# Kernel optimization log

Measured on AMD Instinct MI355X. Metric: run time of the kernel, lower is better.

The kernel has to match this reference:

```python
import jax, jax.numpy as jnp
import numpy as np

B, N, DIM, H = 32, 3136, 768, 12
C = DIM // H  # head_dim = 64


def setup_inputs() -> dict:
    key = jax.random.key(0)
    k1, k2, k3, k4 = jax.random.split(key, 4)
    x = jax.random.normal(k1, (B, N, DIM), dtype=jnp.float32)
    # Linear weights stored as (in, out); qkv has no bias (qkv_bias=False)
    w_qkv = jax.random.normal(k2, (DIM, 3 * DIM), dtype=jnp.float32) * (1.0 / np.sqrt(DIM))
    w_proj = jax.random.normal(k3, (DIM, DIM), dtype=jnp.float32) * (1.0 / np.sqrt(DIM))
    b_proj = jax.random.normal(k4, (DIM,), dtype=jnp.float32) * 0.01
    return {"x": x, "w_qkv": w_qkv, "w_proj": w_proj, "b_proj": b_proj}


def reference(x, w_qkv, w_proj, b_proj):
    # qkv projection: [B,N,3*DIM] -> [3,B,H,N,C]
    qkv = (x @ w_qkv).reshape(B, N, 3, H, C).transpose(2, 0, 3, 1, 4)
    q, k, v = qkv[0], qkv[1], qkv[2]
    # Efficient (linear) attention: softmax q over channel dim, k over token dim
    q = jax.nn.softmax(q, axis=-1)                      # [B,H,N,C], softmax over C
    kt = jax.nn.softmax(k.transpose(0, 1, 3, 2), axis=-1)  # [B,H,C,N], softmax over N
    context = jnp.einsum('bhcn,bhnd->bhcd', kt, v)      # [B,H,C,C]
    out = jnp.einsum('bhnc,bhcd->bhnd', q, context)     # [B,H,N,C]
    out = out.transpose(0, 2, 1, 3).reshape(B, N, DIM)  # [B,N,DIM]
    return out @ w_proj + b_proj
```

## Files before the change

kernel.cpp:

```cpp
#include <hip/hip_runtime.h>
#include <hip/hip_bf16.h>

typedef __attribute__((ext_vector_type(8))) short bf16x8;
typedef __attribute__((ext_vector_type(4))) float f32x4;

constexpr int BATCH = 32, SEQ = 3136, DIM = 768, NH = 12, HD = 64;
constexpr int M_TOT = BATCH * SEQ;
constexpr int QKVC  = 3 * DIM;
constexpr int GK    = 768;

__device__ __forceinline__ float bf2f(unsigned short u) {
  union { unsigned int i; float f; } x; x.i = ((unsigned int)u) << 16; return x.f;
}
__device__ __forceinline__ unsigned short f2bf(float f) {
  union { float f; unsigned int i; } x; x.f = f;
  unsigned int r = x.i + 0x7FFFu + ((x.i >> 16) & 1u);
  return (unsigned short)(r >> 16);
}
__device__ __forceinline__ unsigned int pack2(float lo, float hi) {
  return (unsigned int)f2bf(lo) | ((unsigned int)f2bf(hi) << 16);
}
__device__ __forceinline__ void gload_lds16(const unsigned short* g, unsigned short* l) {
  __builtin_amdgcn_global_load_lds(
      (const __attribute__((address_space(1))) void*)g,
      (__attribute__((address_space(3))) void*)l, 16, 0, 0);
}

#define BARX()  asm volatile("s_barrier" ::: "memory")
#define LGKM0() asm volatile("s_waitcnt lgkmcnt(0)" ::: "memory")
#define VM8()   asm volatile("s_waitcnt vmcnt(8)" ::: "memory")
#define SB0()   __builtin_amdgcn_sched_barrier(0)

__global__ void conv_kernel(const float* __restrict__ in, unsigned short* __restrict__ out, long n) {
  long i = ((long)blockIdx.x * blockDim.x + threadIdx.x) * 8;
  long stride = (long)gridDim.x * blockDim.x * 8;
  for (; i < n; i += stride) {
    float4 a = *(const float4*)(in + i);
    float4 b = *(const float4*)(in + i + 4);
    uint4 o;
    o.x = pack2(a.x, a.y); o.y = pack2(a.z, a.w);
    o.z = pack2(b.x, b.y); o.w = pack2(b.z, b.w);
    *(uint4*)(out + i) = o;
  }
}

__global__ void transp_kernel(const float* __restrict__ w, unsigned short* __restrict__ wt, int K, int N) {
  __shared__ float tile[32][33];
  int n0 = blockIdx.x * 32, k0 = blockIdx.y * 32;
  int tx = threadIdx.x, ty = threadIdx.y;
  #pragma unroll
  for (int i = 0; i < 32; i += 8)
    tile[ty + i][tx] = w[(size_t)(k0 + ty + i) * N + n0 + tx];
  __syncthreads();
  #pragma unroll
  for (int i = 0; i < 32; i += 8)
    wt[(size_t)(n0 + ty + i) * K + k0 + tx] = f2bf(tile[tx][ty + i]);
}

__device__ __forceinline__ void stage_half(const unsigned short* __restrict__ G, long row0, int col0,
                                           unsigned short* ldsHalf, int t) {
  int r = t >> 2;
  int gslot = (t & 3) ^ ((t >> 3) & 3);
  char* dst = (char*)ldsHalf + ((t >> 6) << 10);
  gload_lds16(G + (row0 + r) * (long)GK + col0 + gslot * 8, (unsigned short*)dst);
  gload_lds16(G + (row0 + 128 + r) * (long)GK + col0 + gslot * 8, (unsigned short*)(dst + 8192));
}
__device__ __forceinline__ bf16x8 frag(const unsigned short* half, int r, int ko) {
  return *(const bf16x8*)((const char*)half + r * 64 + ((((ko >> 3) ^ ((r >> 1) & 3))) << 4));
}

#define MM16(Q) do { \
  acc[(Q)*4+0][0]=__builtin_amdgcn_mfma_f32_16x16x32_bf16(a0,b0,acc[(Q)*4+0][0],0,0,0); \
  acc[(Q)*4+0][1]=__builtin_amdgcn_mfma_f32_16x16x32_bf16(a0,b1,acc[(Q)*4+0][1],0,0,0); \
  acc[(Q)*4+0][2]=__builtin_amdgcn_mfma_f32_16x16x32_bf16(a0,b2,acc[(Q)*4+0][2],0,0,0); \
  acc[(Q)*4+0][3]=__builtin_amdgcn_mfma_f32_16x16x32_bf16(a0,b3,acc[(Q)*4+0][3],0,0,0); \
  acc[(Q)*4+1][0]=__builtin_amdgcn_mfma_f32_16x16x32_bf16(a1,b0,acc[(Q)*4+1][0],0,0,0); \
  acc[(Q)*4+1][1]=__builtin_amdgcn_mfma_f32_16x16x32_bf16(a1,b1,acc[(Q)*4+1][1],0,0,0); \
  acc[(Q)*4+1][2]=__builtin_amdgcn_mfma_f32_16x16x32_bf16(a1,b2,acc[(Q)*4+1][2],0,0,0); \
  acc[(Q)*4+1][3]=__builtin_amdgcn_mfma_f32_16x16x32_bf16(a1,b3,acc[(Q)*4+1][3],0,0,0); \
  acc[(Q)*4+2][0]=__builtin_amdgcn_mfma_f32_16x16x32_bf16(a2,b0,acc[(Q)*4+2][0],0,0,0); \
  acc[(Q)*4+2][1]=__builtin_amdgcn_mfma_f32_16x16x32_bf16(a2,b1,acc[(Q)*4+2][1],0,0,0); \
  acc[(Q)*4+2][2]=__builtin_amdgcn_mfma_f32_16x16x32_bf16(a2,b2,acc[(Q)*4+2][2],0,0,0); \
  acc[(Q)*4+2][3]=__builtin_amdgcn_mfma_f32_16x16x32_bf16(a2,b3,acc[(Q)*4+2][3],0,0,0); \
  acc[(Q)*4+3][0]=__builtin_amdgcn_mfma_f32_16x16x32_bf16(a3,b0,acc[(Q)*4+3][0],0,0,0); \
  acc[(Q)*4+3][1]=__builtin_amdgcn_mfma_f32_16x16x32_bf16(a3,b1,acc[(Q)*4+3][1],0,0,0); \
  acc[(Q)*4+3][2]=__builtin_amdgcn_mfma_f32_16x16x32_bf16(a3,b2,acc[(Q)*4+3][2],0,0,0); \
  acc[(Q)*4+3][3]=__builtin_amdgcn_mfma_f32_16x16x32_bf16(a3,b3,acc[(Q)*4+3][3],0,0,0); \
} while (0)

#define KTILE_U(BUF, MA2, NB2, C2, MA3, NB3, C3) { \
  const unsigned short* Ah0 = &lds[BUF][0][0][0]; \
  const unsigned short* Bh0 = &lds[BUF][1][0][0]; \
  const unsigned short* Ah1 = &lds[BUF][0][1][0]; \
  const unsigned short* Bh1 = &lds[BUF][1][1][0]; \
  bf16x8 a0, a1, a2, a3, b0, b1, b2, b3; \
   \
  a0 = frag(Ah0, ra,      ko); a1 = frag(Ah0, ra + 16, ko); \
  a2 = frag(Ah0, ra + 32, ko); a3 = frag(Ah0, ra + 48, ko); \
  b0 = frag(Bh0, rb,      ko); b1 = frag(Bh0, rb + 16, ko); \
  b2 = frag(Bh0, rb + 32, ko); b3 = frag(Bh0, rb + 48, ko); \
  stage_half(A, MA2, C2, &lds[(BUF) ^ 1][0][1][0], t); \
  BARX(); LGKM0(); SB0(); \
  __builtin_amdgcn_s_setprio(1); MM16(0); __builtin_amdgcn_s_setprio(0); BARX(); \
   \
  a0 = frag(Ah0, ra + 64, ko); a1 = frag(Ah0, ra + 80, ko); \
  a2 = frag(Ah0, ra + 96, ko); a3 = frag(Ah0, ra + 112, ko); \
  stage_half(Bt, NB2, C2, &lds[(BUF) ^ 1][1][1][0], t); \
  VM8(); \
  BARX(); LGKM0(); SB0(); \
  __builtin_amdgcn_s_setprio(1); MM16(1); __builtin_amdgcn_s_setprio(0); BARX(); \
   \
  a0 = frag(Ah1, ra,      ko); a1 = frag(Ah1, ra + 16, ko); \
  a2 = frag(Ah1, ra + 32, ko); a3 = frag(Ah1, ra + 48, ko); \
  b0 = frag(Bh1, rb,      ko); b1 = frag(Bh1, rb + 16, ko); \
  b2 = frag(Bh1, rb + 32, ko); b3 = frag(Bh1, rb + 48, ko); \
  stage_half(A, MA3, C3, &lds[BUF][0][0][0], t); \
  BARX(); LGKM0(); SB0(); \
  __builtin_amdgcn_s_setprio(1); MM16(0); __builtin_amdgcn_s_setprio(0); BARX(); \
   \
  a0 = frag(Ah1, ra + 64, ko); a1 = frag(Ah1, ra + 80, ko); \
  a2 = frag(Ah1, ra + 96, ko); a3 = frag(Ah1, ra + 112, ko); \
  stage_half(Bt, NB3, C3, &lds[BUF][1][0][0], t); \
  VM8(); \
  BARX(); LGKM0(); SB0(); \
  __builtin_amdgcn_s_setprio(1); MM16(1); __builtin_amdgcn_s_setprio(0); BARX(); \
}

template<int OUTMODE, int NT>
__global__ __launch_bounds__(512, 2) void gemm256p(const unsigned short* __restrict__ A,
                                                   const unsigned short* __restrict__ Bt,
                                                   void* __restrict__ Cp,
                                                   const float* __restrict__ bias,
                                                   int Nld, int TPX) {
  __shared__ unsigned short lds[2][2][2][8192];
  int t = threadIdx.x, lane = t & 63, wid = t >> 6;
  int wm = wid >> 2, wn = wid & 3;
  int bid = (int)blockIdx.x;
  int xcd = bid & 7, slot = bid >> 3;
  int tau = xcd * TPX + slot;
  int tend = (xcd + 1) * TPX;
  int fl = lane & 15, ko = (lane >> 4) * 8;
  int ra = wm * 128 + fl, rb = wn * 64 + fl;
  f32x4 acc[8][4];
  {
    long m0 = (long)(tau / NT) * 256, n0 = (long)(tau % NT) * 256;
    stage_half(A,  m0, 0,  &lds[0][0][0][0], t);
    stage_half(Bt, n0, 0,  &lds[0][1][0][0], t);
    stage_half(A,  m0, 32, &lds[0][0][1][0], t);
    stage_half(Bt, n0, 32, &lds[0][1][1][0], t);
    stage_half(A,  m0, 64, &lds[1][0][0][0], t);
    stage_half(Bt, n0, 64, &lds[1][1][0][0], t);
    VM8(); BARX();
  }
  #pragma unroll 1
  for (; tau < tend; tau += 32) {
    long m0 = (long)(tau / NT) * 256, n0 = (long)(tau % NT) * 256;
    int tn = (tau + 32 < tend) ? tau + 32 : tau;
    long m0n = (long)(tn / NT) * 256, n0n = (long)(tn % NT) * 256;
    #pragma unroll
    for (int i = 0; i < 8; ++i)
      #pragma unroll
      for (int j2 = 0; j2 < 4; ++j2) acc[i][j2] = (f32x4){0.f, 0.f, 0.f, 0.f};
    #pragma unroll 1
    for (int j = 0; j < 10; j += 2) {
      KTILE_U(0, m0, n0, j * 64 + 96,  m0, n0, j * 64 + 128);
      KTILE_U(1, m0, n0, j * 64 + 160, m0, n0, j * 64 + 192);
    }
    KTILE_U(0, m0,  n0,  736, m0n, n0n, 0);
    KTILE_U(1, m0n, n0n, 32,  m0n, n0n, 64);
    int r0 = (lane >> 4) * 4;
    #pragma unroll
    for (int mf = 0; mf < 8; ++mf) {
      #pragma unroll
      for (int nf = 0; nf < 4; ++nf) {
        long row = m0 + wm * 128 + mf * 16 + r0;
        int col = (int)n0 + wn * 64 + nf * 16 + fl;
        if (OUTMODE == 0) {
          unsigned short* C = (unsigned short*)Cp;
          bool doexp = (n0 < 2 * DIM);
          #pragma unroll
          for (int r = 0; r < 4; ++r) {
            float v = acc[mf][nf][r];
            C[(size_t)(row + r) * Nld + col] = f2bf(doexp ? __expf(v) : v);
          }
        } else {
          float* C = (float*)Cp;
          float bb = bias[col];
          #pragma unroll
          for (int r = 0; r < 4; ++r)
            C[(size_t)(row + r) * Nld + col] = acc[mf][nf][r] + bb;
        }
      }
    }
  }
}

__global__ void ctx_part(const unsigned short* __restrict__ qkv, float* __restrict__ part,
                         float* __restrict__ dpart) {
  int blk = blockIdx.x;
  int bh = blk / 7, ch = blk - bh * 7;
  int b = bh / NH, h = bh % NH;
  __shared__ unsigned short Et[64 * 40];
  __shared__ unsigned short Vt[64 * 40];
  __shared__ float denom[64];
  int t = threadIdx.x, lane = t & 63, w = t >> 6;
  if (t < 64) denom[t] = 0.0f;
  int nl = t >> 3, e0 = (t & 7) * 8;
  int ko = (lane >> 4) * 8, fl = lane & 15;
  size_t base = (size_t)b * SEQ * QKVC + (size_t)h * HD;
  float dp[8] = {};
  f32x4 acc[4] = {};
  int c0b = ch * 448;
  for (int c0 = c0b; c0 < c0b + 448; c0 += 32) {
    __syncthreads();
    size_t rb = base + (size_t)(c0 + nl) * QKVC;
    uint4 kvec = *(const uint4*)(qkv + rb + DIM + e0);
    uint4 vvec = *(const uint4*)(qkv + rb + 2 * DIM + e0);
    const unsigned short* kp = (const unsigned short*)&kvec;
    const unsigned short* vp = (const unsigned short*)&vvec;
    #pragma unroll
    for (int j = 0; j < 8; ++j) {
      dp[j] += bf2f(kp[j]);
      Et[(e0 + j) * 40 + nl] = kp[j];
      Vt[(e0 + j) * 40 + nl] = vp[j];
    }
    __syncthreads();
    bf16x8 af = *(const bf16x8*)(Et + (w * 16 + fl) * 40 + ko);
    #pragma unroll
    for (int nf = 0; nf < 4; ++nf) {
      bf16x8 bv = *(const bf16x8*)(Vt + (nf * 16 + fl) * 40 + ko);
      acc[nf] = __builtin_amdgcn_mfma_f32_16x16x32_bf16(af, bv, acc[nf], 0, 0, 0);
    }
  }
  #pragma unroll
  for (int j = 0; j < 8; ++j) atomicAdd(&denom[e0 + j], dp[j]);
  __syncthreads();
  int r0 = (lane >> 4) * 4;
  float* pp = part + (size_t)blk * 4096;
  #pragma unroll
  for (int nf = 0; nf < 4; ++nf)
    #pragma unroll
    for (int r = 0; r < 4; ++r) {
      int c = w * 16 + r0 + r;
      int d = nf * 16 + fl;
      pp[d * 64 + c] = acc[nf][r];
    }
  if (t < 64) dpart[blk * 64 + t] = denom[t];
}

__global__ void ctx_reduce(const float* __restrict__ part, const float* __restrict__ dpart,
                           unsigned short* __restrict__ ctxT) {
  int bh = blockIdx.x, t = threadIdx.x;
  const float* pp = part + (size_t)bh * 7 * 4096;
  const float* dd = dpart + (size_t)bh * 7 * 64;
  #pragma unroll
  for (int i = 0; i < 16; ++i) {
    int idx = i * 256 + t;
    float s = 0.f, ds = 0.f;
    #pragma unroll
    for (int c = 0; c < 7; ++c) {
      s += pp[c * 4096 + idx];
      ds += dd[c * 64 + (idx & 63)];
    }
    ctxT[(size_t)bh * 4096 + idx] = f2bf(s / ds);
  }
}

__global__ void pv_kernel(const unsigned short* __restrict__ qkv, const unsigned short* __restrict__ ctxT,
                          unsigned short* __restrict__ aout) {
  int bid = blockIdx.x;
  int bh = bid / 49, chunk = bid - bh * 49;
  int b = bh / NH, h = bh % NH;
  int n0 = chunk * 64;
  __shared__ unsigned short P[64 * 80];
  __shared__ unsigned short CT[64 * 80];
  __shared__ float srow[64];
  int t = threadIdx.x, lane = t & 63, w = t >> 6;
  int ko = (lane >> 4) * 8, fl = lane & 15;
  if (t < 64) srow[t] = 0.0f;
  {
    int d = t >> 2, cq = (t & 3) * 16;
    const uint4* src = (const uint4*)(ctxT + (size_t)bh * 4096 + d * 64 + cq);
    *(uint4*)(CT + d * 80 + cq) = src[0];
    *(uint4*)(CT + d * 80 + cq + 8) = src[1];
  }
  __syncthreads();
  {
    int nl = t >> 2, cq = (t & 3) * 16;
    size_t rb = (size_t)(b * SEQ + n0 + nl) * QKVC + h * HD + cq;
    uint4 q0 = *(const uint4*)(qkv + rb);
    uint4 q1 = *(const uint4*)(qkv + rb + 8);
    *(uint4*)(P + nl * 80 + cq) = q0;
    *(uint4*)(P + nl * 80 + cq + 8) = q1;
    const unsigned short* qp0 = (const unsigned short*)&q0;
    const unsigned short* qp1 = (const unsigned short*)&q1;
    float s = 0.0f;
    #pragma unroll
    for (int j = 0; j < 8; ++j) s += bf2f(qp0[j]) + bf2f(qp1[j]);
    atomicAdd(&srow[nl], s);
  }
  __syncthreads();
  f32x4 acc[4] = {};
  #pragma unroll
  for (int kk = 0; kk < 2; ++kk) {
    bf16x8 af = *(const bf16x8*)(P + (w * 16 + fl) * 80 + kk * 32 + ko);
    #pragma unroll
    for (int nf = 0; nf < 4; ++nf) {
      bf16x8 bv = *(const bf16x8*)(CT + (nf * 16 + fl) * 80 + kk * 32 + ko);
      acc[nf] = __builtin_amdgcn_mfma_f32_16x16x32_bf16(af, bv, acc[nf], 0, 0, 0);
    }
  }
  int r0 = (lane >> 4) * 4;
  #pragma unroll
  for (int nf = 0; nf < 4; ++nf)
    #pragma unroll
    for (int r = 0; r < 4; ++r) {
      int nlr = w * 16 + r0 + r;
      int d = nf * 16 + fl;
      float v = acc[nf][r] / srow[nlr];
      aout[(size_t)(b * SEQ + n0 + nlr) * DIM + h * HD + d] = f2bf(v);
    }
}

extern "C" void kernel_launch(void* const* d_in, const int* in_sizes, int n_in,
                              void* d_out, int out_size, void* d_ws, size_t ws_size,
                              hipStream_t stream) {
  const float* x      = (const float*)d_in[0];
  const float* w_qkv  = (const float*)d_in[1];
  const float* w_proj = (const float*)d_in[2];
  const float* b_proj = (const float*)d_in[3];
  char* ws = (char*)d_ws;
  unsigned short* x_bf    = (unsigned short*)(ws);
  unsigned short* wt_qkv  = (unsigned short*)(ws + 154140672);
  unsigned short* wt_proj = (unsigned short*)(ws + 157679616);
  unsigned short* qkv     = (unsigned short*)(ws + 158859264);
  unsigned short* ctxT    = (unsigned short*)(ws + 154140672);
  float* part  = (float*)(ws);
  float* dpart = (float*)(ws + 44040192);
  unsigned short* aout = (unsigned short*)(ws);

  conv_kernel<<<2048, 256, 0, stream>>>(x, x_bf, (long)M_TOT * DIM);
  transp_kernel<<<dim3(QKVC / 32, DIM / 32), dim3(32, 8), 0, stream>>>(w_qkv, wt_qkv, DIM, QKVC);
  transp_kernel<<<dim3(DIM / 32, DIM / 32), dim3(32, 8), 0, stream>>>(w_proj, wt_proj, DIM, DIM);
  gemm256p<0, 9><<<256, 512, 0, stream>>>(x_bf, wt_qkv, qkv, nullptr, QKVC, 441);
  ctx_part<<<BATCH * NH * 7, 256, 0, stream>>>(qkv, part, dpart);
  ctx_reduce<<<BATCH * NH, 256, 0, stream>>>(part, dpart, ctxT);
  pv_kernel<<<BATCH * NH * (SEQ / 64), 256, 0, stream>>>(qkv, ctxT, aout);
  gemm256p<1, 3><<<256, 512, 0, stream>>>(aout, wt_proj, (float*)d_out, b_proj, DIM, 147);
}
```

Before: 810.7 us.

## Double-buffer MFMA operand fragments in registers to overlap LDS reads with compute

Restructures the GEMM k-tile macro into a software-pipelined schedule. Each MFMA block runs on fragments loaded in the previous phase while the next fragments are read from LDS, using a second register set (a4-a7, b4-b7). Barriers drop from two per phase to one, and the vmcnt waits change from 8 to 4 outstanding loads. This targets LDS-read latency and barrier stalls between MFMA groups, at the cost of more vector registers, which could cause spills or lower occupancy under launch_bounds(512,2).

```diff
diff --git a/kernel.cpp b/kernel.cpp
--- a/kernel.cpp
+++ b/kernel.cpp
@@ -29,6 +29,7 @@
 #define BARX()  asm volatile("s_barrier" ::: "memory")
 #define LGKM0() asm volatile("s_waitcnt lgkmcnt(0)" ::: "memory")
 #define VM8()   asm volatile("s_waitcnt vmcnt(8)" ::: "memory")
+#define VM4()   asm volatile("s_waitcnt vmcnt(4)" ::: "memory")
 #define SB0()   __builtin_amdgcn_sched_barrier(0)
 
 __global__ void conv_kernel(const float* __restrict__ in, unsigned short* __restrict__ out, long n) {
@@ -69,61 +70,64 @@
   return *(const bf16x8*)((const char*)half + r * 64 + ((((ko >> 3) ^ ((r >> 1) & 3))) << 4));
 }
 
-#define MM16(Q) do { \
-  acc[(Q)*4+0][0]=__builtin_amdgcn_mfma_f32_16x16x32_bf16(a0,b0,acc[(Q)*4+0][0],0,0,0); \
-  acc[(Q)*4+0][1]=__builtin_amdgcn_mfma_f32_16x16x32_bf16(a0,b1,acc[(Q)*4+0][1],0,0,0); \
-  acc[(Q)*4+0][2]=__builtin_amdgcn_mfma_f32_16x16x32_bf16(a0,b2,acc[(Q)*4+0][2],0,0,0); \
-  acc[(Q)*4+0][3]=__builtin_amdgcn_mfma_f32_16x16x32_bf16(a0,b3,acc[(Q)*4+0][3],0,0,0); \
-  acc[(Q)*4+1][0]=__builtin_amdgcn_mfma_f32_16x16x32_bf16(a1,b0,acc[(Q)*4+1][0],0,0,0); \
-  acc[(Q)*4+1][1]=__builtin_amdgcn_mfma_f32_16x16x32_bf16(a1,b1,acc[(Q)*4+1][1],0,0,0); \
-  acc[(Q)*4+1][2]=__builtin_amdgcn_mfma_f32_16x16x32_bf16(a1,b2,acc[(Q)*4+1][2],0,0,0); \
-  acc[(Q)*4+1][3]=__builtin_amdgcn_mfma_f32_16x16x32_bf16(a1,b3,acc[(Q)*4+1][3],0,0,0); \
-  acc[(Q)*4+2][0]=__builtin_amdgcn_mfma_f32_16x16x32_bf16(a2,b0,acc[(Q)*4+2][0],0,0,0); \
-  acc[(Q)*4+2][1]=__builtin_amdgcn_mfma_f32_16x16x32_bf16(a2,b1,acc[(Q)*4+2][1],0,0,0); \
-  acc[(Q)*4+2][2]=__builtin_amdgcn_mfma_f32_16x16x32_bf16(a2,b2,acc[(Q)*4+2][2],0,0,0); \
-  acc[(Q)*4+2][3]=__builtin_amdgcn_mfma_f32_16x16x32_bf16(a2,b3,acc[(Q)*4+2][3],0,0,0); \
-  acc[(Q)*4+3][0]=__builtin_amdgcn_mfma_f32_16x16x32_bf16(a3,b0,acc[(Q)*4+3][0],0,0,0); \
-  acc[(Q)*4+3][1]=__builtin_amdgcn_mfma_f32_16x16x32_bf16(a3,b1,acc[(Q)*4+3][1],0,0,0); \
-  acc[(Q)*4+3][2]=__builtin_amdgcn_mfma_f32_16x16x32_bf16(a3,b2,acc[(Q)*4+3][2],0,0,0); \
-  acc[(Q)*4+3][3]=__builtin_amdgcn_mfma_f32_16x16x32_bf16(a3,b3,acc[(Q)*4+3][3],0,0,0); \
+#define MM16G(Q,A0,A1,A2,A3,B0,B1,B2,B3) do { \
+  acc[(Q)+0][0]=__builtin_amdgcn_mfma_f32_16x16x32_bf16(A0,B0,acc[(Q)+0][0],0,0,0); \
+  acc[(Q)+0][1]=__builtin_amdgcn_mfma_f32_16x16x32_bf16(A0,B1,acc[(Q)+0][1],0,0,0); \
+  acc[(Q)+0][2]=__builtin_amdgcn_mfma_f32_16x16x32_bf16(A0,B2,acc[(Q)+0][2],0,0,0); \
+  acc[(Q)+0][3]=__builtin_amdgcn_mfma_f32_16x16x32_bf16(A0,B3,acc[(Q)+0][3],0,0,0); \
+  acc[(Q)+1][0]=__builtin_amdgcn_mfma_f32_16x16x32_bf16(A1,B0,acc[(Q)+1][0],0,0,0); \
+  acc[(Q)+1][1]=__builtin_amdgcn_mfma_f32_16x16x32_bf16(A1,B1,acc[(Q)+1][1],0,0,0); \
+  acc[(Q)+1][2]=__builtin_amdgcn_mfma_f32_16x16x32_bf16(A1,B2,acc[(Q)+1][2],0,0,0); \
+  acc[(Q)+1][3]=__builtin_amdgcn_mfma_f32_16x16x32_bf16(A1,B3,acc[(Q)+1][3],0,0,0); \
+  acc[(Q)+2][0]=__builtin_amdgcn_mfma_f32_16x16x32_bf16(A2,B0,acc[(Q)+2][0],0,0,0); \
+  acc[(Q)+2][1]=__builtin_amdgcn_mfma_f32_16x16x32_bf16(A2,B1,acc[(Q)+2][1],0,0,0); \
+  acc[(Q)+2][2]=__builtin_amdgcn_mfma_f32_16x16x32_bf16(A2,B2,acc[(Q)+2][2],0,0,0); \
+  acc[(Q)+2][3]=__builtin_amdgcn_mfma_f32_16x16x32_bf16(A2,B3,acc[(Q)+2][3],0,0,0); \
+  acc[(Q)+3][0]=__builtin_amdgcn_mfma_f32_16x16x32_bf16(A3,B0,acc[(Q)+3][0],0,0,0); \
+  acc[(Q)+3][1]=__builtin_amdgcn_mfma_f32_16x16x32_bf16(A3,B1,acc[(Q)+3][1],0,0,0); \
+  acc[(Q)+3][2]=__builtin_amdgcn_mfma_f32_16x16x32_bf16(A3,B2,acc[(Q)+3][2],0,0,0); \
+  acc[(Q)+3][3]=__builtin_amdgcn_mfma_f32_16x16x32_bf16(A3,B3,acc[(Q)+3][3],0,0,0); \
 } while (0)
 
-#define KTILE_U(BUF, MA2, NB2, C2, MA3, NB3, C3) { \
+#define KTILE_P(BUF, MA2, NB2, C2, MA3, NB3, C3) { \
   const unsigned short* Ah0 = &lds[BUF][0][0][0]; \
   const unsigned short* Bh0 = &lds[BUF][1][0][0]; \
   const unsigned short* Ah1 = &lds[BUF][0][1][0]; \
   const unsigned short* Bh1 = &lds[BUF][1][1][0]; \
-  bf16x8 a0, a1, a2, a3, b0, b1, b2, b3; \
+  const unsigned short* Ah0n = &lds[(BUF) ^ 1][0][0][0]; \
+  const unsigned short* Bh0n = &lds[(BUF) ^ 1][1][0][0]; \
    \
-  a0 = frag(Ah0, ra,      ko); a1 = frag(Ah0, ra + 16, ko); \
-  a2 = frag(Ah0, ra + 32, ko); a3 = frag(Ah0, ra + 48, ko); \
-  b0 = frag(Bh0, rb,      ko); b1 = frag(Bh0, rb + 16, ko); \
-  b2 = frag(Bh0, rb + 32, ko); b3 = frag(Bh0, rb + 48, ko); \
+  LGKM0(); SB0(); VM4(); \
+  a4 = frag(Ah0, ra + 64, ko); a5 = frag(Ah0, ra + 80, ko); \
+  a6 = frag(Ah0, ra + 96, ko); a7 = frag(Ah0, ra + 112, ko); \
   stage_half(A, MA2, C2, &lds[(BUF) ^ 1][0][1][0], t); \
-  BARX(); LGKM0(); SB0(); \
-  __builtin_amdgcn_s_setprio(1); MM16(0); __builtin_amdgcn_s_setprio(0); BARX(); \
+  __builtin_amdgcn_s_setprio(1); MM16G(0, a0, a1, a2, a3, b0, b1, b2, b3); \
+  __builtin_amdgcn_s_setprio(0); SB0(); BARX(); \
    \
-  a0 = frag(Ah0, ra + 64, ko); a1 = frag(Ah0, ra + 80, ko); \
-  a2 = frag(Ah0, ra + 96, ko); a3 = frag(Ah0, ra + 112, ko); \
-  stage_half(Bt, NB2, C2, &lds[(BUF) ^ 1][1][1][0], t); \
-  VM8(); \
-  BARX(); LGKM0(); SB0(); \
-  __builtin_amdgcn_s_setprio(1); MM16(1); __builtin_amdgcn_s_setprio(0); BARX(); \
-   \
+  LGKM0(); SB0(); \
   a0 = frag(Ah1, ra,      ko); a1 = frag(Ah1, ra + 16, ko); \
   a2 = frag(Ah1, ra + 32, ko); a3 = frag(Ah1, ra + 48, ko); \
-  b0 = frag(Bh1, rb,      ko); b1 = frag(Bh1, rb + 16, ko); \
-  b2 = frag(Bh1, rb + 32, ko); b3 = frag(Bh1, rb + 48, ko); \
+  b4 = frag(Bh1, rb,      ko); b5 = frag(Bh1, rb + 16, ko); \
+  b6 = frag(Bh1, rb + 32, ko); b7 = frag(Bh1, rb + 48, ko); \
+  stage_half(Bt, NB2, C2, &lds[(BUF) ^ 1][1][1][0], t); \
+  __builtin_amdgcn_s_setprio(1); MM16G(4, a4, a5, a6, a7, b0, b1, b2, b3); \
+  __builtin_amdgcn_s_setprio(0); SB0(); BARX(); \
+   \
+  LGKM0(); SB0(); VM4(); \
+  a4 = frag(Ah1, ra + 64, ko); a5 = frag(Ah1, ra + 80, ko); \
+  a6 = frag(Ah1, ra + 96, ko); a7 = frag(Ah1, ra + 112, ko); \
   stage_half(A, MA3, C3, &lds[BUF][0][0][0], t); \
-  BARX(); LGKM0(); SB0(); \
-  __builtin_amdgcn_s_setprio(1); MM16(0); __builtin_amdgcn_s_setprio(0); BARX(); \
+  __builtin_amdgcn_s_setprio(1); MM16G(0, a0, a1, a2, a3, b4, b5, b6, b7); \
+  __builtin_amdgcn_s_setprio(0); SB0(); BARX(); \
    \
-  a0 = frag(Ah1, ra + 64, ko); a1 = frag(Ah1, ra + 80, ko); \
-  a2 = frag(Ah1, ra + 96, ko); a3 = frag(Ah1, ra + 112, ko); \
+  LGKM0(); SB0(); \
+  a0 = frag(Ah0n, ra,      ko); a1 = frag(Ah0n, ra + 16, ko); \
+  a2 = frag(Ah0n, ra + 32, ko); a3 = frag(Ah0n, ra + 48, ko); \
+  b0 = frag(Bh0n, rb,      ko); b1 = frag(Bh0n, rb + 16, ko); \
+  b2 = frag(Bh0n, rb + 32, ko); b3 = frag(Bh0n, rb + 48, ko); \
   stage_half(Bt, NB3, C3, &lds[BUF][1][0][0], t); \
-  VM8(); \
-  BARX(); LGKM0(); SB0(); \
-  __builtin_amdgcn_s_setprio(1); MM16(1); __builtin_amdgcn_s_setprio(0); BARX(); \
+  __builtin_amdgcn_s_setprio(1); MM16G(4, a4, a5, a6, a7, b4, b5, b6, b7); \
+  __builtin_amdgcn_s_setprio(0); SB0(); BARX(); \
 }
 
 template<int OUTMODE, int NT>
@@ -142,6 +146,7 @@
   int fl = lane & 15, ko = (lane >> 4) * 8;
   int ra = wm * 128 + fl, rb = wn * 64 + fl;
   f32x4 acc[8][4];
+  bf16x8 a0, a1, a2, a3, a4, a5, a6, a7, b0, b1, b2, b3, b4, b5, b6, b7;
   {
     long m0 = (long)(tau / NT) * 256, n0 = (long)(tau % NT) * 256;
     stage_half(A,  m0, 0,  &lds[0][0][0][0], t);
@@ -151,6 +156,10 @@
     stage_half(A,  m0, 64, &lds[1][0][0][0], t);
     stage_half(Bt, n0, 64, &lds[1][1][0][0], t);
     VM8(); BARX();
+    a0 = frag(&lds[0][0][0][0], ra,      ko); a1 = frag(&lds[0][0][0][0], ra + 16, ko);
+    a2 = frag(&lds[0][0][0][0], ra + 32, ko); a3 = frag(&lds[0][0][0][0], ra + 48, ko);
+    b0 = frag(&lds[0][1][0][0], rb,      ko); b1 = frag(&lds[0][1][0][0], rb + 16, ko);
+    b2 = frag(&lds[0][1][0][0], rb + 32, ko); b3 = frag(&lds[0][1][0][0], rb + 48, ko);
   }
   #pragma unroll 1
   for (; tau < tend; tau += 32) {
@@ -163,11 +172,11 @@
       for (int j2 = 0; j2 < 4; ++j2) acc[i][j2] = (f32x4){0.f, 0.f, 0.f, 0.f};
     #pragma unroll 1
     for (int j = 0; j < 10; j += 2) {
-      KTILE_U(0, m0, n0, j * 64 + 96,  m0, n0, j * 64 + 128);
-      KTILE_U(1, m0, n0, j * 64 + 160, m0, n0, j * 64 + 192);
-    }
-    KTILE_U(0, m0,  n0,  736, m0n, n0n, 0);
-    KTILE_U(1, m0n, n0n, 32,  m0n, n0n, 64);
+      KTILE_P(0, m0, n0, j * 64 + 96,  m0, n0, j * 64 + 128);
+      KTILE_P(1, m0, n0, j * 64 + 160, m0, n0, j * 64 + 192);
+    }
+    KTILE_P(0, m0,  n0,  736, m0n, n0n, 0);
+    KTILE_P(1, m0n, n0n, 32,  m0n, n0n, 64);
     int r0 = (lane >> 4) * 4;
     #pragma unroll
     for (int mf = 0; mf < 8; ++mf) {
```

Measured after the change: 908.8 us. +12.1%, slower.
